# Optimization experiments

Hardware: AMD Instinct MI355X
Metric: run time of the kernel (lower is better)

Reference implementation:

```python
import jax, jax.numpy as jnp
import numpy as np

# SH constants (standard 3DGS eval_sh, degree 3)
C0 = 0.28209479177387814
C1 = 0.4886025119029199
C2 = (1.0925484305920792, -1.0925484305920792, 0.31539156525252005, -1.0925484305920792, 0.5462742152960396)
C3 = (-0.5900435899266435, 2.890611442640554, -0.4570457994644658, 0.3731763325901154, -0.4570457994644658, 1.445305721320277, -0.5900435899266435)

N_GAUSS = 4096
N_PTS = 32768
CHUNK = 4096  # math-identical to torch's 16384 chunking (pure concat of independent points)


def quat_to_rot(q):
    # q: (N,4) normalized, (w,x,y,z) as in 3DGS build_rotation
    r, x, y, z = q[:, 0], q[:, 1], q[:, 2], q[:, 3]
    R = jnp.stack([
        jnp.stack([1 - 2 * (y * y + z * z), 2 * (x * y - r * z), 2 * (x * z + r * y)], -1),
        jnp.stack([2 * (x * y + r * z), 1 - 2 * (x * x + z * z), 2 * (y * z - r * x)], -1),
        jnp.stack([2 * (x * z - r * y), 2 * (y * z + r * x), 1 - 2 * (x * x + y * y)], -1),
    ], axis=-2)  # (N,3,3)
    return R


def eval_sh3(sh, dirs):
    # sh: (N,16) scalar SH coeffs; dirs: (C,N,3) unit directions -> (C,N)
    x, y, z = dirs[..., 0], dirs[..., 1], dirs[..., 2]
    xx, yy, zz = x * x, y * y, z * z
    xy, yz, xz = x * y, y * z, x * z
    s = sh[None]  # (1,N,16)
    res = C0 * s[..., 0]
    res = res - C1 * y * s[..., 1] + C1 * z * s[..., 2] - C1 * x * s[..., 3]
    res = (res + C2[0] * xy * s[..., 4] + C2[1] * yz * s[..., 5]
           + C2[2] * (2 * zz - xx - yy) * s[..., 6]
           + C2[3] * xz * s[..., 7] + C2[4] * (xx - yy) * s[..., 8])
    res = (res + C3[0] * y * (3 * xx - yy) * s[..., 9] + C3[1] * xy * z * s[..., 10]
           + C3[2] * y * (4 * zz - xx - yy) * s[..., 11]
           + C3[3] * z * (2 * zz - 3 * xx - 3 * yy) * s[..., 12]
           + C3[4] * x * (4 * zz - xx - yy) * s[..., 13]
           + C3[5] * z * (xx - yy) * s[..., 14]
           + C3[6] * x * (xx - yy - 3 * zz) * s[..., 15])
    return res


def setup_inputs() -> dict:
    key = jax.random.key(0)
    ks = jax.random.split(key, 9)
    return {
        "network_pts": jax.random.normal(ks[0], (N_PTS, 3), jnp.float32),
        "network_view": jax.random.normal(ks[1], (N_PTS, 3), jnp.float32),
        "network_tx": jax.random.normal(ks[2], (N_PTS, 3), jnp.float32),
        "xyz": jax.random.normal(ks[3], (N_GAUSS, 3), jnp.float32),
        "sh_dc": jax.random.normal(ks[4], (N_GAUSS, 1), jnp.float32),
        "sh_rest": 0.1 * jax.random.normal(ks[5], (N_GAUSS, 15), jnp.float32),
        "scaling": jnp.float32(-3.0) + 0.2 * jax.random.normal(ks[6], (N_GAUSS, 3), jnp.float32),
        "rotation": jax.random.normal(ks[7], (N_GAUSS, 4), jnp.float32),
        "opacity_logit": jax.random.normal(ks[8], (N_GAUSS, 1), jnp.float32),
    }


def reference(network_pts, network_view, network_tx, xyz, sh_dc, sh_rest, scaling, rotation, opacity_logit):
    # activations, matching GaussianModel.setup_functions
    sh = jnp.concatenate([sh_dc, sh_rest], axis=1)            # (N,16)
    s = jnp.exp(scaling)                                      # (N,3)
    q = rotation / jnp.linalg.norm(rotation, axis=1, keepdims=True)
    R = quat_to_rot(q)                                        # (N,3,3)
    # precision = (L L^T)^{-1} with L = R diag(s)  =>  R diag(1/s^2) R^T
    prec = jnp.einsum('nij,nj,nkj->nik', R, 1.0 / (s * s), R)  # (N,3,3)
    op = jax.nn.sigmoid(opacity_logit)[:, 0]                  # (N,)

    pts = network_pts.reshape(-1, CHUNK, 3)

    def chunk_fn(p):  # p: (C,3)
        diff = p[:, None, :] - xyz[None, :, :]                # (C,N,3)
        maha = jnp.einsum('cni,nij,cnj->cn', diff, prec, diff)
        w = op[None, :] * jnp.exp(-0.5 * maha)                # (C,N)
        # dir_pp = xyz - query_point, normalized (as in get_magnitude)
        dirs = -diff / jnp.linalg.norm(diff, axis=-1, keepdims=True)
        mag = jnp.maximum(eval_sh3(sh, dirs), 0.0)            # (C,N)
        return w.sum(axis=1), (w * mag).sum(axis=1)

    opac_c, sig_c = jax.lax.map(chunk_fn, pts)
    return opac_c.reshape(-1), sig_c.reshape(-1)
```

## Files before the change

### kernel.cpp

```cpp
#include <hip/hip_runtime.h>
#include <hip/hip_bf16.h>

#define N_GAUSS 4096
#define N_PTS   32768
#define BLOCK   256
#define NCHUNK  32
#define NBLK_PT 128
#define GSTRIDE 32
#define NCELL   4096
#define NBIN    32
#define RECCAP  128

#define SH_C0  0.28209479177387814f
#define SH_C1  0.4886025119029199f

#define WS_GP     0
#define WS_GHIST  131072
#define WS_CELLID 135168
#define WS_SPTS   167936
#define WS_ACC    299008
#define WS_HPART  364544
#define WS_ACT    495616
#define WS_NACT   1019904

__device__ __forceinline__ int cell_of(float x, float y, float z) {
    int cx = min(15, max(0, (int)((x + 3.2f) * 2.5f)));
    int cy = min(15, max(0, (int)((y + 3.2f) * 2.5f)));
    int cz = min(15, max(0, (int)((z + 3.2f) * 2.5f)));
    int ex = (cx & 1) | ((cx & 2) << 2) | ((cx & 4) << 4) | ((cx & 8) << 6);
    int ey = (cy & 1) | ((cy & 2) << 2) | ((cy & 4) << 4) | ((cy & 8) << 6);
    int ez = (cz & 1) | ((cz & 2) << 2) | ((cz & 4) << 4) | ((cz & 8) << 6);
    return ex | (ey << 1) | (ez << 2);
}

__global__ __launch_bounds__(1024) void binprep_kernel(
    const float* __restrict__ pts, const float* __restrict__ xyz,
    const float* __restrict__ sh_dc, const float* __restrict__ sh_rest,
    const float* __restrict__ scaling, const float* __restrict__ rotation,
    const float* __restrict__ opl, float* __restrict__ gp,
    int* __restrict__ cellid, int* __restrict__ hpart, float* __restrict__ acc)
{
    const int t = threadIdx.x, bx = blockIdx.x;

    if (bx >= 36) {
        float4* a4 = (float4*)acc;
        int base = (bx - 36) * 2048 + t;
        a4[base]        = make_float4(0.f, 0.f, 0.f, 0.f);
        a4[base + 1024] = make_float4(0.f, 0.f, 0.f, 0.f);
        return;
    }
    if (bx >= 32) {
        int g = (bx - 32) * 1024 + t;
        float s0 = scaling[3*g+0], s1 = scaling[3*g+1], s2 = scaling[3*g+2];
        float i0 = __expf(-2.0f * s0);
        float i1 = __expf(-2.0f * s1);
        float i2 = __expf(-2.0f * s2);
        float maxs2 = __expf(2.0f * fmaxf(s0, fmaxf(s1, s2)));

        float r = rotation[4*g+0], x = rotation[4*g+1];
        float y = rotation[4*g+2], z = rotation[4*g+3];
        float n = rsqrtf(r*r + x*x + y*y + z*z);
        r *= n; x *= n; y *= n; z *= n;
        float R00 = 1.f - 2.f*(y*y + z*z), R01 = 2.f*(x*y - r*z), R02 = 2.f*(x*z + r*y);
        float R10 = 2.f*(x*y + r*z), R11 = 1.f - 2.f*(x*x + z*z), R12 = 2.f*(y*z - r*x);
        float R20 = 2.f*(x*z - r*y), R21 = 2.f*(y*z + r*x), R22 = 1.f - 2.f*(x*x + y*y);

        float pxx = 0.5f*(R00*R00*i0 + R01*R01*i1 + R02*R02*i2);
        float pxy = 0.5f*(R00*R10*i0 + R01*R11*i1 + R02*R12*i2);
        float pxz = 0.5f*(R00*R20*i0 + R01*R21*i1 + R02*R22*i2);
        float pyy = 0.5f*(R10*R10*i0 + R11*R11*i1 + R12*R12*i2);
        float pyz = 0.5f*(R10*R20*i0 + R11*R21*i1 + R12*R22*i2);
        float pzz = 0.5f*(R20*R20*i0 + R21*R21*i1 + R22*R22*i2);

        float op   = 1.f / (1.f + __expf(-opl[g]));
        float lnop = __logf(op);
        float Tg   = 2.0f * maxs2 * (lnop + 16.0f);

        const float* sr = sh_rest + (size_t)g * 15;
        float4* G4 = (float4*)(gp + (size_t)g * GSTRIDE);
        G4[0] = make_float4(xyz[3*g+0], xyz[3*g+1], xyz[3*g+2], Tg);
        G4[1] = make_float4(pxx, pxy, pxz, pyy);
        G4[2] = make_float4(pyz, pzz, lnop, 0.f);
        G4[3] = make_float4( SH_C0 * sh_dc[g],
                            -SH_C1 * sr[0],
                             SH_C1 * sr[1],
                            -SH_C1 * sr[2]);
        G4[4] = make_float4( 1.0925484305920792f  * sr[3],
                            -1.0925484305920792f  * sr[4],
                             0.31539156525252005f * sr[5],
                            -1.0925484305920792f  * sr[6]);
        G4[5] = make_float4( 0.5462742152960396f  * sr[7],
                            -0.5900435899266435f  * sr[8],
                             2.890611442640554f   * sr[9],
                            -0.4570457994644658f  * sr[10]);
        G4[6] = make_float4( 0.3731763325901154f  * sr[11],
                            -0.4570457994644658f  * sr[12],
                             1.445305721320277f   * sr[13],
                            -0.5900435899266435f  * sr[14]);
        G4[7] = make_float4(0.f, 0.f, 0.f, 0.f);
        return;
    }

    __shared__ int s_hist[NCELL];
    #pragma unroll
    for (int i = 0; i < 4; ++i) s_hist[t + i * 1024] = 0;
    __syncthreads();
    {
        int p = bx * 1024 + t;
        float x = pts[3*p+0], y = pts[3*p+1], z = pts[3*p+2];
        int cell = cell_of(x, y, z);
        cellid[p] = cell;
        atomicAdd(&s_hist[cell], 1);
    }
    __syncthreads();
    #pragma unroll
    for (int i = 0; i < 4; ++i) {
        int c = t + i * 1024;
        hpart[bx * NCELL + c] = s_hist[c];
    }
}

__global__ __launch_bounds__(1024) void scan_kernel(
    const int* __restrict__ hpart, int* __restrict__ ghist)
{
    __shared__ int s_wsum[16];
    const int t = threadIdx.x;
    const int lane = t & 63, wv = t >> 6;
    const int b = t * 4;

    int4 c = make_int4(0, 0, 0, 0);
    #pragma unroll
    for (int k = 0; k < NBIN; ++k) {
        int4 h = *(const int4*)(hpart + k * NCELL + b);
        c.x += h.x; c.y += h.y; c.z += h.z; c.w += h.w;
    }
    int s = c.x + c.y + c.z + c.w;

    int incl = s;
    #pragma unroll
    for (int off = 1; off < 64; off <<= 1) {
        int v = __shfl_up(incl, off);
        if (lane >= off) incl += v;
    }
    if (lane == 63) s_wsum[wv] = incl;
    __syncthreads();
    if (wv == 0) {
        int ws = (lane < 16) ? s_wsum[lane] : 0;
        int wincl = ws;
        #pragma unroll
        for (int off = 1; off < 16; off <<= 1) {
            int v = __shfl_up(wincl, off);
            if (lane >= off) wincl += v;
        }
        if (lane < 16) s_wsum[lane] = wincl - ws;
    }
    __syncthreads();

    int excl = s_wsum[wv] + (incl - s);
    ghist[b]   = excl;
    ghist[b+1] = excl + c.x;
    ghist[b+2] = excl + c.x + c.y;
    ghist[b+3] = excl + c.x + c.y + c.z;
}

__global__ __launch_bounds__(256) void scatter_kernel(
    const float* __restrict__ pts, const int* __restrict__ cellid,
    int* __restrict__ ghist, float4* __restrict__ spts)
{
    int p = blockIdx.x * 256 + threadIdx.x;
    float x = pts[3*p+0], y = pts[3*p+1], z = pts[3*p+2];
    int pos = atomicAdd(&ghist[cellid[p]], 1);
    spts[pos] = make_float4(x, y, z, __int_as_float(p));
}

__global__ __launch_bounds__(BLOCK) void cull_kernel(
    const float4* __restrict__ spts, const float4* __restrict__ gp4,
    int* __restrict__ actlist, int* __restrict__ nactg)
{
    __shared__ float s_min[4][3], s_max[4][3];
    __shared__ int s_n;
    __shared__ int s_list[N_GAUSS];

    const int tid = threadIdx.x;
    const int pb  = blockIdx.x;
    float4 P = spts[pb * 256 + tid];
    const float px = P.x, py = P.y, pz = P.z;

    float mnx = px, mxx = px, mny = py, mxy = py, mnz = pz, mxz = pz;
    #pragma unroll
    for (int off = 32; off >= 1; off >>= 1) {
        mnx = fminf(mnx, __shfl_xor(mnx, off));
        mxx = fmaxf(mxx, __shfl_xor(mxx, off));
        mny = fminf(mny, __shfl_xor(mny, off));
        mxy = fmaxf(mxy, __shfl_xor(mxy, off));
        mnz = fminf(mnz, __shfl_xor(mnz, off));
        mxz = fmaxf(mxz, __shfl_xor(mxz, off));
    }
    const int wave = tid >> 6;
    if ((tid & 63) == 0) {
        s_min[wave][0] = mnx; s_min[wave][1] = mny; s_min[wave][2] = mnz;
        s_max[wave][0] = mxx; s_max[wave][1] = mxy; s_max[wave][2] = mxz;
    }
    if (tid == 0) s_n = 0;
    __syncthreads();
    const float bmnx = fminf(fminf(s_min[0][0], s_min[1][0]), fminf(s_min[2][0], s_min[3][0]));
    const float bmny = fminf(fminf(s_min[0][1], s_min[1][1]), fminf(s_min[2][1], s_min[3][1]));
    const float bmnz = fminf(fminf(s_min[0][2], s_min[1][2]), fminf(s_min[2][2], s_min[3][2]));
    const float bmxx = fmaxf(fmaxf(s_max[0][0], s_max[1][0]), fmaxf(s_max[2][0], s_max[3][0]));
    const float bmxy = fmaxf(fmaxf(s_max[0][1], s_max[1][1]), fmaxf(s_max[2][1], s_max[3][1]));
    const float bmxz = fmaxf(fmaxf(s_max[0][2], s_max[1][2]), fmaxf(s_max[2][2], s_max[3][2]));

    for (int r = 0; r < N_GAUSS / BLOCK; ++r) {
        const int gg = r * BLOCK + tid;
        float4 c = gp4[(size_t)gg << 3];
        float ddx = fmaxf(0.f, fmaxf(bmnx - c.x, c.x - bmxx));
        float ddy = fmaxf(0.f, fmaxf(bmny - c.y, c.y - bmxy));
        float ddz = fmaxf(0.f, fmaxf(bmnz - c.z, c.z - bmxz));
        float dd2 = ddx*ddx + ddy*ddy + ddz*ddz;
        if (dd2 <= c.w) {
            int slot = atomicAdd(&s_n, 1);
            s_list[slot] = gg;
        }
    }
    __syncthreads();
    const int n = s_n;
    for (int i = tid; i < n; i += BLOCK) actlist[pb * N_GAUSS + i] = s_list[i];
    if (tid == 0) nactg[pb] = n;
}

__device__ __forceinline__ void eval_one(
    const float4* R, float dx, float dy, float dz, float d2,
    float& opac, float& sig)
{
    float4 q1 = R[1], q2 = R[2];
    float vx = q1.x*dx + q1.y*dy + q1.z*dz;
    float vy = q1.y*dx + q1.w*dy + q2.x*dz;
    float vz = q1.z*dx + q2.x*dy + q2.y*dz;
    float maha = dx*vx + dy*vy + dz*vz;
    float w = __expf(q2.z - maha);
    opac += w;

    if (__any(w > 1e-9f)) {
        float4 q3 = R[3], q4 = R[4], q5 = R[5], q6 = R[6];
        float rinv = rsqrtf(d2);
        float x = -dx * rinv, y = -dy * rinv, z = -dz * rinv;
        float xx = x*x, yy = y*y, zz = z*z;
        float xy = x*y, yz = y*z, xz = x*z;

        float res = q3.x;
        res += y * q3.y;
        res += z * q3.z;
        res += x * q3.w;
        res += xy * q4.x;
        res += yz * q4.y;
        res += (3.f*zz - 1.f) * q4.z;
        res += xz * q4.w;
        float xxmyy = xx - yy;
        res += xxmyy * q5.x;
        res += y * (3.f*xx - yy) * q5.y;
        res += (xy * z) * q5.z;
        float f5z1 = 5.f*zz - 1.f;
        res += y * f5z1 * q5.w;
        res += z * (5.f*zz - 3.f) * q6.x;
        res += x * f5z1 * q6.y;
        res += z * xxmyy * q6.z;
        res += x * (xxmyy - 3.f*zz) * q6.w;

        sig += w * fmaxf(res, 0.f);
    }
}

__global__ __launch_bounds__(BLOCK) void eval_kernel(
    const float4* __restrict__ spts, const float4* __restrict__ gp4,
    const int* __restrict__ actlist, const int* __restrict__ nactg,
    float* __restrict__ acc)
{
    __shared__ int s_idx[RECCAP];
    __shared__ float4 s_rec[RECCAP * 8];

    const int tid = threadIdx.x;
    const int ck  = blockIdx.x;
    const int pb  = blockIdx.y;

    const int nact = nactg[pb];
    const int c0 = (nact * ck) / NCHUNK;
    const int c1 = (nact * (ck + 1)) / NCHUNK;
    const int cnt = c1 - c0;
    if (cnt == 0) return;

    float4 P = spts[pb * 256 + tid];
    if (tid < cnt) s_idx[tid] = actlist[pb * N_GAUSS + c0 + tid];
    __syncthreads();

    for (int idx = tid; idx < cnt * 8; idx += BLOCK) {
        int rec = idx >> 3, q = idx & 7;
        s_rec[idx] = gp4[((size_t)s_idx[rec] << 3) + q];
    }
    __syncthreads();

    const float px = P.x, py = P.y, pz = P.z;
    float opac = 0.f, sig = 0.f;
    for (int j = 0; j < cnt; j += 2) {
        const bool has1 = (j + 1 < cnt);
        const float4* A = &s_rec[j * 8];
        const float4* B = &s_rec[(has1 ? j + 1 : j) * 8];

        float4 aq0 = A[0];
        float4 bq0 = B[0];
        float adx = px - aq0.x, ady = py - aq0.y, adz = pz - aq0.z;
        float bdx = px - bq0.x, bdy = py - bq0.y, bdz = pz - bq0.z;
        float ad2 = adx*adx + ady*ady + adz*adz;
        float bd2 = bdx*bdx + bdy*bdy + bdz*bdz;

        if (!__all(ad2 > aq0.w)) eval_one(A, adx, ady, adz, ad2, opac, sig);
        if (has1 && !__all(bd2 > bq0.w)) eval_one(B, bdx, bdy, bdz, bd2, opac, sig);
    }

    const int pos = pb * 256 + tid;
    atomicAdd(&acc[pos], opac);
    atomicAdd(&acc[N_PTS + pos], sig);
}

__global__ __launch_bounds__(256) void permute_kernel(
    const float* __restrict__ acc, const float4* __restrict__ spts,
    float* __restrict__ out)
{
    int p = blockIdx.x * 256 + threadIdx.x;
    int orig = __float_as_int(spts[p].w);
    out[orig] = acc[p];
    out[N_PTS + orig] = acc[N_PTS + p];
}

extern "C" void kernel_launch(void* const* d_in, const int* in_sizes, int n_in,
                              void* d_out, int out_size, void* d_ws, size_t ws_size,
                              hipStream_t stream) {
    const float* pts      = (const float*)d_in[0];
    const float* xyz      = (const float*)d_in[3];
    const float* sh_dc    = (const float*)d_in[4];
    const float* sh_rest  = (const float*)d_in[5];
    const float* scaling  = (const float*)d_in[6];
    const float* rotation = (const float*)d_in[7];
    const float* opl      = (const float*)d_in[8];

    float*  out     = (float*)d_out;
    float*  wsf     = (float*)d_ws;
    float*  gp      = wsf + WS_GP;
    int*    ghist   = (int*)(wsf + WS_GHIST);
    int*    cellid  = (int*)(wsf + WS_CELLID);
    float4* spts    = (float4*)(wsf + WS_SPTS);
    float*  acc     = wsf + WS_ACC;
    int*    hpart   = (int*)(wsf + WS_HPART);
    int*    actlist = (int*)(wsf + WS_ACT);
    int*    nactg   = (int*)(wsf + WS_NACT);

    binprep_kernel<<<dim3(44), dim3(1024), 0, stream>>>(
        pts, xyz, sh_dc, sh_rest, scaling, rotation, opl, gp, cellid, hpart, acc);
    scan_kernel<<<dim3(1), dim3(1024), 0, stream>>>(hpart, ghist);
    scatter_kernel<<<dim3(NBLK_PT), dim3(256), 0, stream>>>(pts, cellid, ghist, spts);

    cull_kernel<<<dim3(NBLK_PT), dim3(BLOCK), 0, stream>>>(
        spts, (const float4*)gp, actlist, nactg);
    eval_kernel<<<dim3(NCHUNK, NBLK_PT), dim3(BLOCK), 0, stream>>>(
        spts, (const float4*)gp, actlist, nactg, acc);
    permute_kernel<<<dim3(NBLK_PT), dim3(256), 0, stream>>>(acc, spts, out);
}
```

Before: 123.2 us.

## Halve histogram bins, drop shared index staging, unroll eval loop by four

The histogram pass now uses 16 bin blocks, each processing 2048 points instead of 1024, which shrinks the partial-histogram buffer and the scan work. The eval kernel no longer stages actlist indices in shared memory; it reads them directly from global memory during the record gather, removing one barrier. The inner Gaussian loop is unrolled by four with a scalar tail instead of pairs, to expose more independent work per iteration. Register pressure may rise and the per-block histogram pass gets longer.

```diff
diff --git a/kernel.cpp b/kernel.cpp
--- a/kernel.cpp
+++ b/kernel.cpp
@@ -8,7 +8,7 @@
 #define NBLK_PT 128
 #define GSTRIDE 32
 #define NCELL   4096
-#define NBIN    32
+#define NBIN    16
 #define RECCAP  128
 
 #define SH_C0  0.28209479177387814f
@@ -20,8 +20,8 @@
 #define WS_SPTS   167936
 #define WS_ACC    299008
 #define WS_HPART  364544
-#define WS_ACT    495616
-#define WS_NACT   1019904
+#define WS_ACT    430080
+#define WS_NACT   954368
 
 __device__ __forceinline__ int cell_of(float x, float y, float z) {
     int cx = min(15, max(0, (int)((x + 3.2f) * 2.5f)));
@@ -42,15 +42,15 @@
 {
     const int t = threadIdx.x, bx = blockIdx.x;
 
-    if (bx >= 36) {
+    if (bx >= 20) {
         float4* a4 = (float4*)acc;
-        int base = (bx - 36) * 2048 + t;
+        int base = (bx - 20) * 2048 + t;
         a4[base]        = make_float4(0.f, 0.f, 0.f, 0.f);
         a4[base + 1024] = make_float4(0.f, 0.f, 0.f, 0.f);
         return;
     }
-    if (bx >= 32) {
-        int g = (bx - 32) * 1024 + t;
+    if (bx >= 16) {
+        int g = (bx - 16) * 1024 + t;
         float s0 = scaling[3*g+0], s1 = scaling[3*g+1], s2 = scaling[3*g+2];
         float i0 = __expf(-2.0f * s0);
         float i1 = __expf(-2.0f * s1);
@@ -105,8 +105,9 @@
     #pragma unroll
     for (int i = 0; i < 4; ++i) s_hist[t + i * 1024] = 0;
     __syncthreads();
-    {
-        int p = bx * 1024 + t;
+    #pragma unroll
+    for (int k = 0; k < 2; ++k) {
+        int p = bx * 2048 + k * 1024 + t;
         float x = pts[3*p+0], y = pts[3*p+1], z = pts[3*p+2];
         int cell = cell_of(x, y, z);
         cellid[p] = cell;
@@ -275,7 +276,6 @@
     const int* __restrict__ actlist, const int* __restrict__ nactg,
     float* __restrict__ acc)
 {
-    __shared__ int s_idx[RECCAP];
     __shared__ float4 s_rec[RECCAP * 8];
 
     const int tid = threadIdx.x;
@@ -289,31 +289,43 @@
     if (cnt == 0) return;
 
     float4 P = spts[pb * 256 + tid];
-    if (tid < cnt) s_idx[tid] = actlist[pb * N_GAUSS + c0 + tid];
-    __syncthreads();
+    const int* alist = actlist + pb * N_GAUSS + c0;
 
     for (int idx = tid; idx < cnt * 8; idx += BLOCK) {
         int rec = idx >> 3, q = idx & 7;
-        s_rec[idx] = gp4[((size_t)s_idx[rec] << 3) + q];
+        s_rec[idx] = gp4[((size_t)alist[rec] << 3) + q];
     }
     __syncthreads();
 
     const float px = P.x, py = P.y, pz = P.z;
     float opac = 0.f, sig = 0.f;
-    for (int j = 0; j < cnt; j += 2) {
-        const bool has1 = (j + 1 < cnt);
-        const float4* A = &s_rec[j * 8];
-        const float4* B = &s_rec[(has1 ? j + 1 : j) * 8];
-
-        float4 aq0 = A[0];
-        float4 bq0 = B[0];
-        float adx = px - aq0.x, ady = py - aq0.y, adz = pz - aq0.z;
-        float bdx = px - bq0.x, bdy = py - bq0.y, bdz = pz - bq0.z;
+    int j = 0;
+    for (; j + 4 <= cnt; j += 4) {
+        const float4* R0 = &s_rec[(j + 0) * 8];
+        const float4* R1 = &s_rec[(j + 1) * 8];
+        const float4* R2 = &s_rec[(j + 2) * 8];
+        const float4* R3 = &s_rec[(j + 3) * 8];
+        float4 a = R0[0], b = R1[0], c = R2[0], d = R3[0];
+        float adx = px - a.x, ady = py - a.y, adz = pz - a.z;
+        float bdx = px - b.x, bdy = py - b.y, bdz = pz - b.z;
+        float cdx = px - c.x, cdy = py - c.y, cdz = pz - c.z;
+        float ddx = px - d.x, ddy = py - d.y, ddz = pz - d.z;
         float ad2 = adx*adx + ady*ady + adz*adz;
         float bd2 = bdx*bdx + bdy*bdy + bdz*bdz;
-
-        if (!__all(ad2 > aq0.w)) eval_one(A, adx, ady, adz, ad2, opac, sig);
-        if (has1 && !__all(bd2 > bq0.w)) eval_one(B, bdx, bdy, bdz, bd2, opac, sig);
+        float cd2 = cdx*cdx + cdy*cdy + cdz*cdz;
+        float dd2 = ddx*ddx + ddy*ddy + ddz*ddz;
+
+        if (!__all(ad2 > a.w)) eval_one(R0, adx, ady, adz, ad2, opac, sig);
+        if (!__all(bd2 > b.w)) eval_one(R1, bdx, bdy, bdz, bd2, opac, sig);
+        if (!__all(cd2 > c.w)) eval_one(R2, cdx, cdy, cdz, cd2, opac, sig);
+        if (!__all(dd2 > d.w)) eval_one(R3, ddx, ddy, ddz, dd2, opac, sig);
+    }
+    for (; j < cnt; ++j) {
+        const float4* R0 = &s_rec[j * 8];
+        float4 a = R0[0];
+        float adx = px - a.x, ady = py - a.y, adz = pz - a.z;
+        float ad2 = adx*adx + ady*ady + adz*adz;
+        if (!__all(ad2 > a.w)) eval_one(R0, adx, ady, adz, ad2, opac, sig);
     }
 
     const int pos = pb * 256 + tid;
@@ -353,7 +365,7 @@
     int*    actlist = (int*)(wsf + WS_ACT);
     int*    nactg   = (int*)(wsf + WS_NACT);
 
-    binprep_kernel<<<dim3(44), dim3(1024), 0, stream>>>(
+    binprep_kernel<<<dim3(28), dim3(1024), 0, stream>>>(
         pts, xyz, sh_dc, sh_rest, scaling, rotation, opl, gp, cellid, hpart, acc);
     scan_kernel<<<dim3(1), dim3(1024), 0, stream>>>(hpart, ghist);
     scatter_kernel<<<dim3(NBLK_PT), dim3(256), 0, stream>>>(pts, cellid, ghist, spts);
```

New measurement: 119.9 us. 2.7% less time.
